# Performance work log

Measured on AMD Instinct MI355X. Metric: run time of the kernel, lower is better.

Reference implementation:

```python
import jax, jax.numpy as jnp
import numpy as np

B, T, O, H = 64, 1000, 61, 256
IN0, IN1 = 320, 2 * H  # layer0 input = 8*40 flattened feats; layer1 input = bidirectional concat


def setup_inputs() -> dict:
    key = jax.random.key(0)
    ks = jax.random.split(key, 12)
    rn = lambda k, shape: (jax.random.normal(k, shape, dtype=jnp.float32) * 0.05)
    inp = {}
    inp["batch"] = jax.random.normal(ks[0], (B, T, 8, 40), dtype=jnp.float32)
    lengths = np.random.RandomState(0).randint(T // 2, T + 1, size=B).astype(np.int64)
    inp["lengths"] = jnp.asarray(lengths)
    # GRU params stacked over directions: [2, 3H, in], [2, 3H, H], biases [2, 3H]
    inp["w_ih_l0"] = rn(ks[1], (2, 3 * H, IN0))
    inp["w_hh_l0"] = rn(ks[2], (2, 3 * H, H))
    inp["b_ih_l0"] = rn(ks[3], (2, 3 * H))
    inp["b_hh_l0"] = rn(ks[4], (2, 3 * H))
    inp["w_ih_l1"] = rn(ks[5], (2, 3 * H, IN1))
    inp["w_hh_l1"] = rn(ks[6], (2, 3 * H, H))
    inp["b_ih_l1"] = rn(ks[7], (2, 3 * H))
    inp["b_hh_l1"] = rn(ks[8], (2, 3 * H))
    inp["fc_w"] = rn(ks[9], (O, 2 * H))
    inp["fc_b"] = rn(ks[10], (O,))
    return inp


def _gru_dir(x, w_ih, w_hh, b_ih, b_hh, reverse):
    # x: [T, B, in] -> ys: [T, B, H]; torch GRU cell semantics
    def step(h, xt):
        gi = xt @ w_ih.T + b_ih          # [B, 3H]
        gh = h @ w_hh.T + b_hh           # [B, 3H]
        i_r, i_z, i_n = jnp.split(gi, 3, axis=-1)
        h_r, h_z, h_n = jnp.split(gh, 3, axis=-1)
        r = jax.nn.sigmoid(i_r + h_r)
        z = jax.nn.sigmoid(i_z + h_z)
        n = jnp.tanh(i_n + r * h_n)
        h_new = (1.0 - z) * n + z * h
        return h_new, h_new
    h0 = jnp.zeros((x.shape[1], w_hh.shape[-1]), x.dtype)
    _, ys = jax.lax.scan(step, h0, x, reverse=reverse)
    return ys


def _bigru_layer(x, w_ih, w_hh, b_ih, b_hh):
    fwd = _gru_dir(x, w_ih[0], w_hh[0], b_ih[0], b_hh[0], reverse=False)
    bwd = _gru_dir(x, w_ih[1], w_hh[1], b_ih[1], b_hh[1], reverse=True)
    return jnp.concatenate([fwd, bwd], axis=-1)  # [T, B, 2H]


def reference(batch, lengths, w_ih_l0, w_hh_l0, b_ih_l0, b_hh_l0,
              w_ih_l1, w_hh_l1, b_ih_l1, b_hh_l1, fc_w, fc_b):
    b, t = batch.shape[0], batch.shape[1]
    x = jnp.swapaxes(batch, 2, 3).reshape(b, t, -1)   # transpose(2,3).flatten(2) -> [B,T,320]
    x = jnp.swapaxes(x, 0, 1)                          # [T, B, 320] (time-major like torch GRU)
    h1 = _bigru_layer(x, w_ih_l0, w_hh_l0, b_ih_l0, b_hh_l0)
    h2 = _bigru_layer(h1, w_ih_l1, w_hh_l1, b_ih_l1, b_hh_l1)
    out = h2 @ fc_w.T + fc_b                           # [T, B, O]
    out = jnp.swapaxes(out, 0, 1)                      # [B, T, O]
    # gather first lengths[i] timesteps of each sample, concatenated
    L = np.asarray(lengths)
    mask = np.arange(t)[None, :] < L[:, None]
    bi, ti = np.nonzero(mask)
    return out[bi, ti]                                 # [sum(lengths), O]
```

## Files before the change

### kernel.cpp

```cpp
#include <hip/hip_runtime.h>
#include <cstdint>
#include <cstddef>


typedef __attribute__((ext_vector_type(8))) __bf16 bf16x8;
typedef __attribute__((ext_vector_type(4))) float f32x4;
typedef __attribute__((ext_vector_type(4))) unsigned int u32x4;

#define AS1 __attribute__((address_space(1)))
#define AS3 __attribute__((address_space(3)))

#define LOG2E 1.44269504089f
#define SRZ  (-1.44269504089f)
#define SN   (2.88539008177f)

__device__ __forceinline__ void async_ld16(const void* g, void* l) {
  __builtin_amdgcn_global_load_lds((const AS1 unsigned int*)g,
                                   (AS3 unsigned int*)l, 16, 0, 0);
}

__device__ __forceinline__ f32x4 mfma16(u32x4 a, u32x4 b, f32x4 c) {
  return __builtin_amdgcn_mfma_f32_16x16x32_bf16(
      __builtin_bit_cast(bf16x8, a), __builtin_bit_cast(bf16x8, b), c, 0, 0, 0);
}

__device__ __forceinline__ unsigned short f2b(float f) {
  unsigned int u = __float_as_uint(f);
  u += 0x7fffu + ((u >> 16) & 1u);
  return (unsigned short)(u >> 16);
}
__device__ __forceinline__ float b2f(unsigned short s) {
  return __uint_as_float(((unsigned int)s) << 16);
}
__device__ __forceinline__ unsigned int cvtpk(float lo, float hi) {
  unsigned int r;
  asm("v_cvt_pk_bf16_f32 %0, %1, %2" : "=v"(r) : "v"(lo), "v"(hi));
  return r;
}
__device__ __forceinline__ float lo16(unsigned int d) {
  return __uint_as_float(d << 16);
}
__device__ __forceinline__ float hi16(unsigned int d) {
  return __uint_as_float(d & 0xffff0000u);
}
__device__ __forceinline__ float gload(const float* p, size_t i) { return p[i]; }
__device__ __forceinline__ float gload(const unsigned short* p, size_t i) { return b2f(p[i]); }

__device__ __forceinline__ float sigm2(float xs) {
  return __builtin_amdgcn_rcpf(1.0f + __builtin_amdgcn_exp2f(xs));
}
__device__ __forceinline__ float tanh2(float ys) {
  return __builtin_fmaf(-2.0f,
      __builtin_amdgcn_rcpf(1.0f + __builtin_amdgcn_exp2f(ys)), 1.0f);
}

__device__ __forceinline__ void lds_barrier() {
  asm volatile("" ::: "memory");
  __builtin_amdgcn_s_waitcnt(0xC07F);
  __builtin_amdgcn_s_barrier();
  asm volatile("" ::: "memory");
}

__global__ void cast_bf16_kernel(const float* __restrict__ src,
                                 unsigned short* __restrict__ dst, int n) {
  const int i = blockIdx.x * 256 + threadIdx.x;
  if (i < n) dst[i] = f2b(src[i]);
}

__global__ void cast_w_kernel(const float* __restrict__ src,
                              unsigned short* __restrict__ dst, int n,
                              int in_dim) {
  const int i = blockIdx.x * 256 + threadIdx.x;
  if (i < n) {
    const int row = (i / in_dim) % 768;
    const float s = (row < 512) ? SRZ : SN;
    dst[i] = f2b(s * src[i]);
  }
}

__global__ void cast_w_perm_kernel(const float* __restrict__ src,
                                   unsigned short* __restrict__ dst, int n,
                                   int in_dim, int scaled) {
  const int i = blockIdx.x * 256 + threadIdx.x;
  if (i < n) {
    const int row = i / in_dim;
    const int p = i - row * in_dim;
    const int hi = p >> 8, pr = p & 255;
    const int w = pr >> 5, c2 = pr & 31;
    const int k = hi * 256 + w * 32 + (c2 & 1) * 16 + (c2 >> 1);
    float s = 1.0f;
    if (scaled) s = ((row % 768) < 512) ? SRZ : SN;
    dst[i] = f2b(s * src[(size_t)row * in_dim + k]);
  }
}

__global__ void bias_fuse_kernel(const float* __restrict__ bih,
                                 const float* __restrict__ bhh,
                                 float* __restrict__ fb) {
  const int n = blockIdx.x * 256 + threadIdx.x;
  if (n < 1536) {
    const int dir = n >> 9 >> 1 ? 1 : (n / 768);
    const int rr = n - dir * 768;
    const float s = (rr < 512) ? SRZ : SN;
    float v = bih[dir * 768 + rr];
    if (rr < 512) v += bhh[dir * 768 + rr];
    fb[n] = s * v;
  }
}

__global__ void transpose_x_kernel(const float* __restrict__ batch,
                                   unsigned short* __restrict__ xb) {
  const int t = blockIdx.x, b = blockIdx.y, i = threadIdx.x;
  const float v = batch[((size_t)b * 1000 + t) * 320 + (i & 7) * 40 + (i >> 3)];
  xb[((size_t)t * 64 + b) * 320 + i] = f2b(v);
}

template <typename CT, bool PERM>
__global__ __launch_bounds__(256) void gemm_bt_kernel(
    const unsigned short* __restrict__ A, const unsigned short* __restrict__ W,
    const float* __restrict__ bias, CT* __restrict__ C, int M, int N, int K) {
  __shared__ __align__(16) unsigned short As[4096];
  __shared__ __align__(16) unsigned short Bs[4096];
  const int tid = threadIdx.x;
  const int lane = tid & 63;
  const int wv = tid >> 6;
  const int mBase = blockIdx.x * 128;
  const int nBase = blockIdx.y * 128;

  const int s0 = tid, s1 = tid + 256;
  const int r0 = ((s0 >> 6) << 4) | (s0 & 15), c0 = ((s0 >> 4) & 3) * 8;
  const int r1 = ((s1 >> 6) << 4) | (s1 & 15), c1 = ((s1 >> 4) & 3) * 8;

  const unsigned short* Arow0 = A + (size_t)(mBase + r0) * K + c0;
  const unsigned short* Arow1 = A + (size_t)(mBase + r1) * K + c1;
  const unsigned short* Wrow0 = W + (size_t)(nBase + r0) * K + c0;
  const unsigned short* Wrow1 = W + (size_t)(nBase + r1) * K + c1;

  char* lA = (char*)As;
  char* lB = (char*)Bs;
  char* dstA0 = lA + wv * 1024;
  char* dstA1 = lA + 4096 + wv * 1024;
  char* dstB0 = lB + wv * 1024;
  char* dstB1 = lB + 4096 + wv * 1024;

  f32x4 acc[4][4] = {};
  const int mh = (wv >> 1) * 64, nh = (wv & 1) * 64;
  const u32x4* As4 = (const u32x4*)As;
  const u32x4* Bs4 = (const u32x4*)Bs;

  for (int k0 = 0; k0 < K; k0 += 32) {
    __syncthreads();
    async_ld16(Arow0 + k0, dstA0);
    async_ld16(Arow1 + k0, dstA1);
    async_ld16(Wrow0 + k0, dstB0);
    async_ld16(Wrow1 + k0, dstB1);
    __syncthreads();
    u32x4 a[4], b[4];
#pragma unroll
    for (int mt = 0; mt < 4; ++mt) a[mt] = As4[((mh >> 4) + mt) * 64 + lane];
#pragma unroll
    for (int nt = 0; nt < 4; ++nt) b[nt] = Bs4[((nh >> 4) + nt) * 64 + lane];
#pragma unroll
    for (int mt = 0; mt < 4; ++mt)
#pragma unroll
      for (int nt = 0; nt < 4; ++nt)
        acc[mt][nt] = mfma16(a[mt], b[nt], acc[mt][nt]);
  }

  if constexpr (PERM) {
    const int t = (mBase + mh) >> 6;
#pragma unroll
    for (int p = 0; p < 2; ++p) {
      const int nb0 = nBase + nh + p * 32;
      const int dir = (nb0 >= 768) ? 1 : 0;
      const int np = nb0 - dir * 768;
      const int g = np >> 8;
      const int ww = (np >> 5) & 7;
      const float bn0 = bias[nb0 + (lane & 15)];
      const float bn1 = bias[nb0 + 16 + (lane & 15)];
#pragma unroll
      for (int mt = 0; mt < 4; ++mt) {
        const size_t slot = (size_t)t * 64 + (size_t)(mt * 2 + dir) * 8 + ww;
        if constexpr (sizeof(CT) == 2) {
          u32x4 v;
          v[0] = cvtpk(acc[mt][2 * p][0] + bn0, acc[mt][2 * p][1] + bn0);
          v[1] = cvtpk(acc[mt][2 * p][2] + bn0, acc[mt][2 * p][3] + bn0);
          v[2] = cvtpk(acc[mt][2 * p + 1][0] + bn1, acc[mt][2 * p + 1][1] + bn1);
          v[3] = cvtpk(acc[mt][2 * p + 1][2] + bn1, acc[mt][2 * p + 1][3] + bn1);
          *(u32x4*)((unsigned short*)C + slot * 1536 + (size_t)g * 512 +
                    (size_t)lane * 8) = v;
        } else {
#pragma unroll
          for (int rs = 0; rs < 2; ++rs) {
            f32x4 v = {acc[mt][2 * p][2 * rs] + bn0,
                       acc[mt][2 * p][2 * rs + 1] + bn0,
                       acc[mt][2 * p + 1][2 * rs] + bn1,
                       acc[mt][2 * p + 1][2 * rs + 1] + bn1};
            *(f32x4*)((float*)C + slot * 1536 + (size_t)(g * 2 + rs) * 256 +
                      (size_t)lane * 4) = v;
          }
        }
      }
    }
  } else {
#pragma unroll
    for (int nt = 0; nt < 4; ++nt) {
      const int n = nBase + nh + nt * 16 + (lane & 15);
      const float bn = bias[n];
#pragma unroll
      for (int mt = 0; mt < 4; ++mt) {
        const int mrow = mBase + mh + mt * 16 + ((lane >> 4) << 2);
#pragma unroll
        for (int r = 0; r < 4; ++r) {
          const float v = acc[mt][nt][r] + bn;
          if constexpr (sizeof(CT) == 2)
            ((unsigned short*)C)[(size_t)(mrow + r) * N + n] = f2b(v);
          else
            ((float*)C)[(size_t)(mrow + r) * N + n] = v;
        }
      }
    }
  }
}

#define GBLOCK(G)                                                              \
  {                                                                            \
    _Pragma("unroll") for (int kt = 0; kt < 6; ++kt) {                         \
      acc[0][G] = mfma16(a[kt], wv[0][G][kt], acc[0][G]);                      \
      acc[1][G] = mfma16(a[kt], wv[1][G][kt], acc[1][G]);                      \
    }                                                                          \
    _Pragma("unroll") for (int kk = 0; kk < 2; ++kk) {                         \
      u32x4 bf0 = *(const u32x4*)(wlds +                                       \
          (((w * 12 + (0 * 3 + (G)) * 2 + kk) << 10) + lane * 16));            \
      u32x4 bf1 = *(const u32x4*)(wlds +                                       \
          (((w * 12 + (1 * 3 + (G)) * 2 + kk) << 10) + lane * 16));            \
      acc[0][G] = mfma16(a[6 + kk], bf0, acc[0][G]);                           \
      acc[1][G] = mfma16(a[6 + kk], bf1, acc[1][G]);                           \
    }                                                                          \
  }

template <typename GT>
__global__ __launch_bounds__(512, 2) void gru_fast_kernel(
    const GT* __restrict__ gi,
    const unsigned short* __restrict__ whh,
    const float* __restrict__ bhh,
    unsigned short* __restrict__ hout) {
  constexpr int E = (int)sizeof(GT);
  constexpr int CH = (E * 1536) / 1024;
  constexpr bool DB = (E == 2);
  constexpr int HB = DB ? 18432 : 9216;
  extern __shared__ __align__(16) char smem[];
  char* wlds = smem;
  char* hl   = smem + 98304;
  char* glds = smem + 98304 + HB;
  const int tid = threadIdx.x;
  const int lane = tid & 63;
  const int w = tid >> 6;
  const int c = lane & 15;
  const int q = lane >> 4;
  const int dir = blockIdx.x & 1;
  const int sb = (blockIdx.x >> 1) * 16;

  for (int i = tid; i < HB / 2; i += 512) ((unsigned short*)hl)[i] = 0;

  const int u0 = 32 * w + c;
  const float bhn0 = SN * bhh[dir * 768 + 512 + u0];
  const float bhn1 = SN * bhh[dir * 768 + 512 + u0 + 16];

  const unsigned short* wb =
      whh + (size_t)dir * 196608 + (size_t)u0 * 256 + q * 8;
  u32x4 wv[2][3][6];
#pragma unroll
  for (int j = 0; j < 2; ++j)
#pragma unroll
    for (int g = 0; g < 3; ++g) {
      const unsigned short* p = wb + (size_t)(g * 256 + 16 * j) * 256;
#pragma unroll
      for (int kt = 0; kt < 6; ++kt) wv[j][g][kt] = *(const u32x4*)(p + kt * 32);
#pragma unroll
      for (int kk = 0; kk < 2; ++kk) {
        u32x4 tmp = *(const u32x4*)(p + (6 + kk) * 32);
        *(u32x4*)(wlds + (((w * 12 + (j * 3 + g) * 2 + kk) << 10) + lane * 16)) = tmp;
      }
    }
#pragma unroll
  for (int j = 0; j < 2; ++j)
#pragma unroll
    for (int g = 0; g < 3; ++g)
#pragma unroll
      for (int kt = 0; kt < 6; ++kt)
        asm volatile("" : "+v"(wv[j][g][kt]));

  float h0[4] = {0.f, 0.f, 0.f, 0.f}, h1[4] = {0.f, 0.f, 0.f, 0.f};

  const int t0 = dir ? 999 : 0;
  unsigned int* hp = (unsigned int*)hout +
                     ((size_t)t0 * 64 + sb) * 256 + dir * 128 + w * 16 + c;
  const ptrdiff_t gstep = (dir ? -1 : 1) * (ptrdiff_t)(64 * 1536);
  const ptrdiff_t hstep = (dir ? -1 : 1) * (ptrdiff_t)(64 * 256);

  char* gdw = glds + w * (1536 * E);
  const size_t slot0 =
      (size_t)t0 * 64 + (size_t)((blockIdx.x >> 1) * 2 + dir) * 8 + w;
  const GT* gp2 = gi + slot0 * 1536 + (size_t)lane * (16 / E);
#pragma unroll
  for (int i = 0; i < CH; ++i)
    async_ld16(gp2 + i * (1024 / E), gdw + i * 1024);
  gp2 += gstep;

  __syncthreads();

  const char* habase = hl + c * 576 + q * 16;
  const int hwb = q * 4 * 576 + w * 64 + c * 4;

  auto body = [&](int rd, int wr, bool first) {
    u32x4 a[8];
#pragma unroll
    for (int kt = 0; kt < 8; ++kt)
      a[kt] = *(const u32x4*)(habase + rd + kt * 64);
    if constexpr (!DB) lds_barrier();

    f32x4 acc[2][3] = {};
    GBLOCK(0)

    if (first) asm volatile("s_waitcnt vmcnt(0)" ::: "memory");
    else       asm volatile("s_waitcnt vmcnt(4)" ::: "memory");
    u32x4 raw[CH];
#pragma unroll
    for (int i = 0; i < CH; ++i)
      raw[i] = *(const u32x4*)(gdw + i * 1024 + lane * 16);

    float pvA[3][4], pvB[3][4];
    if constexpr (E == 2) {
#pragma unroll
      for (int g = 0; g < 3; ++g)
#pragma unroll
        for (int r = 0; r < 4; ++r) {
          const unsigned int d0 = raw[g][r >> 1];
          const unsigned int d1 = raw[g][2 + (r >> 1)];
          pvA[g][r] = (r & 1) ? hi16(d0) : lo16(d0);
          pvB[g][r] = (r & 1) ? hi16(d1) : lo16(d1);
        }
    } else {
#pragma unroll
      for (int g = 0; g < 3; ++g)
#pragma unroll
        for (int r = 0; r < 4; ++r) {
          const f32x4 f = __builtin_bit_cast(f32x4, raw[g * 2 + (r >> 1)]);
          pvA[g][r] = f[r & 1];
          pvB[g][r] = f[2 + (r & 1)];
        }
    }

    float rr0[4], rr1[4];
#pragma unroll
    for (int r = 0; r < 4; ++r) {
      rr0[r] = sigm2(pvA[0][r] + acc[0][0][r]);
      rr1[r] = sigm2(pvB[0][r] + acc[1][0][r]);
    }

    GBLOCK(2)

    float nn0[4], nn1[4];
#pragma unroll
    for (int r = 0; r < 4; ++r) {
      nn0[r] = tanh2(__builtin_fmaf(rr0[r], acc[0][2][r] + bhn0, pvA[2][r]));
      nn1[r] = tanh2(__builtin_fmaf(rr1[r], acc[1][2][r] + bhn1, pvB[2][r]));
    }

    GBLOCK(1)

    asm volatile("s_waitcnt lgkmcnt(0)" ::: "memory");
#pragma unroll
    for (int i = 0; i < CH; ++i)
      async_ld16(gp2 + i * (1024 / E), gdw + i * 1024);
    gp2 += gstep;

    unsigned short* hls = (unsigned short*)(hl + wr);
#pragma unroll
    for (int r = 0; r < 4; ++r) {
      const float zz0 = sigm2(pvA[1][r] + acc[0][1][r]);
      const float hv0 = __builtin_fmaf(zz0, h0[r] - nn0[r], nn0[r]);
      h0[r] = hv0;
      const float zz1 = sigm2(pvB[1][r] + acc[1][1][r]);
      const float hv1 = __builtin_fmaf(zz1, h1[r] - nn1[r], nn1[r]);
      h1[r] = hv1;
      const unsigned int pk = cvtpk(hv0, hv1);
      *(unsigned int*)((char*)hls + hwb + r * 576) = pk;
      hp[(size_t)(q * 4 + r) * 256] = pk;
    }
    hp += hstep;
    lds_barrier();
  };

  if constexpr (DB) {
    body(0, 9216, true);
    body(9216, 0, false);
    for (int it = 1; it < 500; ++it) {
      body(0, 9216, false);
      body(9216, 0, false);
    }
  } else {
    body(0, 0, true);
    for (int step = 1; step < 1000; ++step) body(0, 0, false);
  }
  asm volatile("s_waitcnt vmcnt(0)" ::: "memory");
}

template <typename GT>
__global__ __launch_bounds__(1024) void gru_layer_kernel(
    const GT* __restrict__ gi, const unsigned short* __restrict__ whh,
    const float* __restrict__ bhh, unsigned short* __restrict__ hout) {
  __shared__ __align__(16) unsigned short hbf[16][264];
  __shared__ __align__(16) float gh[16][780];
  const int tid = threadIdx.x;
  const int lane = tid & 63;
  const int wv = tid >> 6;
  const int dir = blockIdx.x & 1;
  const int sb = (blockIdx.x >> 1) * 16;
  const int j = tid & 255;
  const int si = tid >> 8;

  float hreg[4] = {0.f, 0.f, 0.f, 0.f};
#pragma unroll
  for (int i = 0; i < 4; ++i) hbf[si + i * 4][j] = 0;

  const float bh_n = SN * bhh[dir * 768 + 512 + j];

  const unsigned short* wl = whh + (size_t)dir * 768 * 256 +
                             (size_t)(wv * 48 + (lane & 15)) * 256 +
                             ((lane >> 4) * 8);
  const char* habase = (const char*)hbf + (lane & 15) * 528 + ((lane >> 4) << 4);
  const int srow = (lane >> 4) * 4;

  __syncthreads();

  for (int step = 0; step < 1000; ++step) {
    const int t = dir ? (999 - step) : step;
    float p_ir[4], p_iz[4], p_in[4];
#pragma unroll
    for (int i = 0; i < 4; ++i) {
      const int s = si + i * 4;
      const size_t gib = ((size_t)t * 64 + (sb + s)) * 1536 + dir * 768 + j;
      p_ir[i] = gload(gi, gib);
      p_iz[i] = gload(gi, gib + 256);
      p_in[i] = gload(gi, gib + 512);
    }
    u32x4 a[8];
#pragma unroll
    for (int kt = 0; kt < 8; ++kt) a[kt] = *(const u32x4*)(habase + kt * 64);
#pragma unroll
    for (int ntd = 0; ntd < 3; ++ntd) {
      f32x4 acc = {0.f, 0.f, 0.f, 0.f};
#pragma unroll
      for (int kt = 0; kt < 8; ++kt) {
        u32x4 bfrag = *(const u32x4*)(wl + ntd * (16 * 256) + kt * 32);
        acc = mfma16(a[kt], bfrag, acc);
      }
      const int gcol = (wv * 3 + ntd) * 16 + (lane & 15);
#pragma unroll
      for (int r = 0; r < 4; ++r) gh[srow + r][gcol] = acc[r];
    }
    __syncthreads();
#pragma unroll
    for (int i = 0; i < 4; ++i) {
      const int s = si + i * 4;
      const float r = sigm2(p_ir[i] + gh[s][j]);
      const float z = sigm2(p_iz[i] + gh[s][256 + j]);
      const float n = tanh2(__builtin_fmaf(r, gh[s][512 + j] + bh_n, p_in[i]));
      const float h = __builtin_fmaf(z, hreg[i] - n, n);
      hreg[i] = h;
      const unsigned short hb = f2b(h);
      hbf[s][j] = hb;
      hout[((size_t)t * 64 + (sb + s)) * 512 + dir * 256 + j] = hb;
    }
    __syncthreads();
  }
}

__global__ void prefix_kernel(const int* __restrict__ raw,
                              int* __restrict__ pref, int* __restrict__ lens) {
  if (threadIdx.x == 0) {
    const int stride = (raw[1] == 0 && raw[3] == 0 && raw[5] == 0) ? 2 : 1;
    int a = 0;
    for (int b = 0; b < 64; ++b) {
      const int L = raw[b * stride];
      pref[b] = a;
      lens[b] = L;
      a += L;
    }
  }
}

__global__ __launch_bounds__(256) void fc_kernel(
    const unsigned short* __restrict__ h2, const unsigned short* __restrict__ fcw,
    const float* __restrict__ fcb, const int* __restrict__ lens,
    const int* __restrict__ pref, float* __restrict__ out) {
  __shared__ __align__(16) unsigned short hrow[4][512];
  const int b = blockIdx.y;
  const int sub = threadIdx.x >> 6, lane = threadIdx.x & 63;
  const int t = blockIdx.x * 4 + sub;
  *(u32x4*)&hrow[sub][lane * 8] =
      *(const u32x4*)&h2[((size_t)t * 64 + b) * 512 + lane * 8];
  __syncthreads();
  const int len = lens[b];
  if (lane < 61 && t < len) {
    float acc = fcb[lane];
    const unsigned short* wr = fcw + (size_t)lane * 512;
#pragma unroll 4
    for (int k = 0; k < 512; k += 8) {
      u32x4 w4 = *(const u32x4*)(wr + k);
      u32x4 h4 = *(const u32x4*)(&hrow[sub][k]);
#pragma unroll
      for (int qq = 0; qq < 4; ++qq) {
        acc += __uint_as_float(w4[qq] << 16) * __uint_as_float(h4[qq] << 16);
        acc += __uint_as_float(w4[qq] & 0xffff0000u) * __uint_as_float(h4[qq] & 0xffff0000u);
      }
    }
    out[((size_t)pref[b] + t) * 61 + lane] = acc;
  }
}

template <typename GT>
static void run_pipeline(const float* batch, const int* lengths_raw,
                         const float* w_ih_l0, const float* w_hh_l0,
                         const float* b_ih_l0, const float* b_hh_l0,
                         const float* w_ih_l1, const float* w_hh_l1,
                         const float* b_ih_l1, const float* b_hh_l1,
                         const float* fc_w, const float* fc_b, float* out,
                         char* ws, hipStream_t stream) {
  size_t off = 0;
  auto alloc = [&](size_t bytes) -> char* {
    char* p = ws + off;
    off += (bytes + 255) & ~(size_t)255;
    return p;
  };
  char* pool = alloc((size_t)64000 * 512 * 2);
  unsigned short* xb = (unsigned short*)pool;
  unsigned short* h1 = (unsigned short*)pool;
  unsigned short* h2 = (unsigned short*)pool;
  GT*             gi   = (GT*)alloc((size_t)64064 * 1536 * sizeof(GT));
  unsigned short* wih0 = (unsigned short*)alloc((size_t)1536 * 320 * 2);
  unsigned short* wih1 = (unsigned short*)alloc((size_t)1536 * 512 * 2);
  unsigned short* whh0 = (unsigned short*)alloc((size_t)1536 * 256 * 2);
  unsigned short* whh1 = (unsigned short*)alloc((size_t)1536 * 256 * 2);
  unsigned short* fcwb = (unsigned short*)alloc((size_t)61 * 512 * 2);
  float*          fb0  = (float*)alloc(1536 * 4);
  float*          fb1  = (float*)alloc(1536 * 4);
  int*            pref = (int*)alloc(256);
  int*            lens = (int*)alloc(256);

  const int HB = (sizeof(GT) == 2) ? 18432 : 9216;
  const int GRU_LDS = 98304 + HB + 8 * 1536 * (int)sizeof(GT);
  const bool big_lds =
      hipFuncSetAttribute(reinterpret_cast<const void*>(gru_fast_kernel<GT>),
                          hipFuncAttributeMaxDynamicSharedMemorySize,
                          GRU_LDS) == hipSuccess;

  auto castw_lin = [&](const float* s, unsigned short* d, int n, int in_dim) {
    cast_w_kernel<<<dim3((n + 255) / 256), dim3(256), 0, stream>>>(s, d, n, in_dim);
  };
  auto castw_perm = [&](const float* s, unsigned short* d, int n, int in_dim,
                        int scaled) {
    cast_w_perm_kernel<<<dim3((n + 255) / 256), dim3(256), 0, stream>>>(
        s, d, n, in_dim, scaled);
  };

  castw_lin(w_ih_l0, wih0, 2 * 768 * 320, 320);
  if (big_lds) {
    castw_perm(w_hh_l0, whh0, 2 * 768 * 256, 256, 1);
    castw_perm(w_hh_l1, whh1, 2 * 768 * 256, 256, 1);
    castw_perm(w_ih_l1, wih1, 2 * 768 * 512, 512, 1);
    castw_perm(fc_w, fcwb, 61 * 512, 512, 0);
  } else {
    castw_lin(w_hh_l0, whh0, 2 * 768 * 256, 256);
    castw_lin(w_hh_l1, whh1, 2 * 768 * 256, 256);
    castw_lin(w_ih_l1, wih1, 2 * 768 * 512, 512);
    cast_bf16_kernel<<<dim3((61 * 512 + 255) / 256), dim3(256), 0, stream>>>(
        fc_w, fcwb, 61 * 512);
  }
  bias_fuse_kernel<<<dim3(6), dim3(256), 0, stream>>>(b_ih_l0, b_hh_l0, fb0);
  bias_fuse_kernel<<<dim3(6), dim3(256), 0, stream>>>(b_ih_l1, b_hh_l1, fb1);

  transpose_x_kernel<<<dim3(1000, 64), dim3(320), 0, stream>>>(batch, xb);

  auto gemm = [&](const unsigned short* A, const unsigned short* W,
                  const float* fb, GT* Cc, int M, int N, int K) {
    if (big_lds)
      gemm_bt_kernel<GT, true><<<dim3(500, 12), dim3(256), 0, stream>>>(
          A, W, fb, Cc, M, N, K);
    else
      gemm_bt_kernel<GT, false><<<dim3(500, 12), dim3(256), 0, stream>>>(
          A, W, fb, Cc, M, N, K);
  };
  auto gru = [&](GT* g, unsigned short* w, const float* b, unsigned short* h) {
    if (big_lds)
      gru_fast_kernel<GT><<<dim3(8), dim3(512), GRU_LDS, stream>>>(g, w, b, h);
    else
      gru_layer_kernel<GT><<<dim3(8), dim3(1024), 0, stream>>>(g, w, b, h);
  };

  gemm(xb, wih0, fb0, gi, 64000, 1536, 320);
  gru(gi, whh0, b_hh_l0, h1);
  gemm(h1, wih1, fb1, gi, 64000, 1536, 512);
  gru(gi, whh1, b_hh_l1, h2);

  prefix_kernel<<<dim3(1), dim3(64), 0, stream>>>(lengths_raw, pref, lens);
  fc_kernel<<<dim3(250, 64), dim3(256), 0, stream>>>(h2, fcwb, fc_b, lens, pref, out);
}

extern "C" void kernel_launch(void* const* d_in, const int* in_sizes, int n_in,
                              void* d_out, int out_size, void* d_ws, size_t ws_size,
                              hipStream_t stream) {
  (void)in_sizes; (void)n_in; (void)out_size;
  const float* batch   = (const float*)d_in[0];
  const int*   lengths = (const int*)d_in[1];
  const float* w_ih_l0 = (const float*)d_in[2];
  const float* w_hh_l0 = (const float*)d_in[3];
  const float* b_ih_l0 = (const float*)d_in[4];
  const float* b_hh_l0 = (const float*)d_in[5];
  const float* w_ih_l1 = (const float*)d_in[6];
  const float* w_hh_l1 = (const float*)d_in[7];
  const float* b_ih_l1 = (const float*)d_in[8];
  const float* b_hh_l1 = (const float*)d_in[9];
  const float* fc_w    = (const float*)d_in[10];
  const float* fc_b    = (const float*)d_in[11];
  float* out = (float*)d_out;
  char* ws = (char*)d_ws;

  const size_t NEED_FP32 = 470000000ull;
  if (ws_size >= NEED_FP32) {
    run_pipeline<float>(batch, lengths, w_ih_l0, w_hh_l0, b_ih_l0, b_hh_l0,
                        w_ih_l1, w_hh_l1, b_ih_l1, b_hh_l1, fc_w, fc_b, out,
                        ws, stream);
  } else {
    run_pipeline<unsigned short>(batch, lengths, w_ih_l0, w_hh_l0, b_ih_l0,
                                 b_hh_l0, w_ih_l1, w_hh_l1, b_ih_l1, b_hh_l1,
                                 fc_w, fc_b, out, ws, stream);
  }
}
```

Measured before the change: 3.637 ms.

## Double-buffer GEMM LDS tiles and seed GRU accumulators with input projections

The input-projection GEMM now uses two LDS buffers, so the next K-slice is prefetched asynchronously while MFMAs run on the current slice, with one barrier per iteration instead of two. In the recurrent GRU step, the z-gate accumulator is initialised with the precomputed input projection and the n-gate accumulator with the hidden bias. This removes the separate adds after the MFMA chain on the serial critical path. The cost is doubled LDS use in the GEMM and a prefetch on the final iteration that reads one slice past K.

```diff
diff --git a/kernel.cpp b/kernel.cpp
--- a/kernel.cpp
+++ b/kernel.cpp
@@ -119,8 +119,8 @@
 __global__ __launch_bounds__(256) void gemm_bt_kernel(
     const unsigned short* __restrict__ A, const unsigned short* __restrict__ W,
     const float* __restrict__ bias, CT* __restrict__ C, int M, int N, int K) {
-  __shared__ __align__(16) unsigned short As[4096];
-  __shared__ __align__(16) unsigned short Bs[4096];
+  __shared__ __align__(16) unsigned short As[2][4096];
+  __shared__ __align__(16) unsigned short Bs[2][4096];
   const int tid = threadIdx.x;
   const int lane = tid & 63;
   const int wv = tid >> 6;
@@ -136,25 +136,27 @@
   const unsigned short* Wrow0 = W + (size_t)(nBase + r0) * K + c0;
   const unsigned short* Wrow1 = W + (size_t)(nBase + r1) * K + c1;
 
-  char* lA = (char*)As;
-  char* lB = (char*)Bs;
-  char* dstA0 = lA + wv * 1024;
-  char* dstA1 = lA + 4096 + wv * 1024;
-  char* dstB0 = lB + wv * 1024;
-  char* dstB1 = lB + 4096 + wv * 1024;
+  auto stage = [&](int buf, int k0) {
+    char* lA = (char*)As[buf];
+    char* lB = (char*)Bs[buf];
+    async_ld16(Arow0 + k0, lA + wv * 1024);
+    async_ld16(Arow1 + k0, lA + 4096 + wv * 1024);
+    async_ld16(Wrow0 + k0, lB + wv * 1024);
+    async_ld16(Wrow1 + k0, lB + 4096 + wv * 1024);
+  };
 
   f32x4 acc[4][4] = {};
   const int mh = (wv >> 1) * 64, nh = (wv & 1) * 64;
-  const u32x4* As4 = (const u32x4*)As;
-  const u32x4* Bs4 = (const u32x4*)Bs;
-
-  for (int k0 = 0; k0 < K; k0 += 32) {
-    __syncthreads();
-    async_ld16(Arow0 + k0, dstA0);
-    async_ld16(Arow1 + k0, dstA1);
-    async_ld16(Wrow0 + k0, dstB0);
-    async_ld16(Wrow1 + k0, dstB1);
-    __syncthreads();
+
+  stage(0, 0);
+  __syncthreads();
+
+  const int NT = K >> 5;
+  for (int t = 0; t < NT; ++t) {
+    const int cur = t & 1;
+    stage(cur ^ 1, (t + 1) << 5);
+    const u32x4* As4 = (const u32x4*)As[cur];
+    const u32x4* Bs4 = (const u32x4*)Bs[cur];
     u32x4 a[4], b[4];
 #pragma unroll
     for (int mt = 0; mt < 4; ++mt) a[mt] = As4[((mh >> 4) + mt) * 64 + lane];
@@ -165,6 +167,7 @@
 #pragma unroll
       for (int nt = 0; nt < 4; ++nt)
         acc[mt][nt] = mfma16(a[mt], b[nt], acc[mt][nt]);
+    __syncthreads();
   }
 
   if constexpr (PERM) {
@@ -320,7 +323,9 @@
       a[kt] = *(const u32x4*)(habase + rd + kt * 64);
     if constexpr (!DB) lds_barrier();
 
-    f32x4 acc[2][3] = {};
+    f32x4 acc[2][3];
+    acc[0][0] = f32x4{0.f, 0.f, 0.f, 0.f};
+    acc[1][0] = f32x4{0.f, 0.f, 0.f, 0.f};
     GBLOCK(0)
 
     if (first) asm volatile("s_waitcnt vmcnt(0)" ::: "memory");
@@ -330,33 +335,44 @@
     for (int i = 0; i < CH; ++i)
       raw[i] = *(const u32x4*)(gdw + i * 1024 + lane * 16);
 
-    float pvA[3][4], pvB[3][4];
+    float pvr0[4], pvr1[4], pvn0[4], pvn1[4];
     if constexpr (E == 2) {
 #pragma unroll
-      for (int g = 0; g < 3; ++g)
-#pragma unroll
-        for (int r = 0; r < 4; ++r) {
-          const unsigned int d0 = raw[g][r >> 1];
-          const unsigned int d1 = raw[g][2 + (r >> 1)];
-          pvA[g][r] = (r & 1) ? hi16(d0) : lo16(d0);
-          pvB[g][r] = (r & 1) ? hi16(d1) : lo16(d1);
-        }
+      for (int r = 0; r < 4; ++r) {
+        const unsigned int dr0 = raw[0][r >> 1], dr1 = raw[0][2 + (r >> 1)];
+        const unsigned int dz0 = raw[1][r >> 1], dz1 = raw[1][2 + (r >> 1)];
+        const unsigned int dn0 = raw[2][r >> 1], dn1 = raw[2][2 + (r >> 1)];
+        pvr0[r] = (r & 1) ? hi16(dr0) : lo16(dr0);
+        pvr1[r] = (r & 1) ? hi16(dr1) : lo16(dr1);
+        acc[0][1][r] = (r & 1) ? hi16(dz0) : lo16(dz0);
+        acc[1][1][r] = (r & 1) ? hi16(dz1) : lo16(dz1);
+        pvn0[r] = (r & 1) ? hi16(dn0) : lo16(dn0);
+        pvn1[r] = (r & 1) ? hi16(dn1) : lo16(dn1);
+        acc[0][2][r] = bhn0;
+        acc[1][2][r] = bhn1;
+      }
     } else {
 #pragma unroll
-      for (int g = 0; g < 3; ++g)
-#pragma unroll
-        for (int r = 0; r < 4; ++r) {
-          const f32x4 f = __builtin_bit_cast(f32x4, raw[g * 2 + (r >> 1)]);
-          pvA[g][r] = f[r & 1];
-          pvB[g][r] = f[2 + (r & 1)];
-        }
+      for (int r = 0; r < 4; ++r) {
+        const f32x4 f0 = __builtin_bit_cast(f32x4, raw[0 + (r >> 1)]);
+        const f32x4 f1 = __builtin_bit_cast(f32x4, raw[2 + (r >> 1)]);
+        const f32x4 f2 = __builtin_bit_cast(f32x4, raw[4 + (r >> 1)]);
+        pvr0[r] = f0[r & 1];
+        pvr1[r] = f0[2 + (r & 1)];
+        acc[0][1][r] = f1[r & 1];
+        acc[1][1][r] = f1[2 + (r & 1)];
+        pvn0[r] = f2[r & 1];
+        pvn1[r] = f2[2 + (r & 1)];
+        acc[0][2][r] = bhn0;
+        acc[1][2][r] = bhn1;
+      }
     }
 
     float rr0[4], rr1[4];
 #pragma unroll
     for (int r = 0; r < 4; ++r) {
-      rr0[r] = sigm2(pvA[0][r] + acc[0][0][r]);
-      rr1[r] = sigm2(pvB[0][r] + acc[1][0][r]);
+      rr0[r] = sigm2(pvr0[r] + acc[0][0][r]);
+      rr1[r] = sigm2(pvr1[r] + acc[1][0][r]);
     }
 
     GBLOCK(2)
@@ -364,8 +380,8 @@
     float nn0[4], nn1[4];
 #pragma unroll
     for (int r = 0; r < 4; ++r) {
-      nn0[r] = tanh2(__builtin_fmaf(rr0[r], acc[0][2][r] + bhn0, pvA[2][r]));
-      nn1[r] = tanh2(__builtin_fmaf(rr1[r], acc[1][2][r] + bhn1, pvB[2][r]));
+      nn0[r] = tanh2(__builtin_fmaf(rr0[r], acc[0][2][r], pvn0[r]));
+      nn1[r] = tanh2(__builtin_fmaf(rr1[r], acc[1][2][r], pvn1[r]));
     }
 
     GBLOCK(1)
@@ -379,10 +395,10 @@
     unsigned short* hls = (unsigned short*)(hl + wr);
 #pragma unroll
     for (int r = 0; r < 4; ++r) {
-      const float zz0 = sigm2(pvA[1][r] + acc[0][1][r]);
+      const float zz0 = sigm2(acc[0][1][r]);
       const float hv0 = __builtin_fmaf(zz0, h0[r] - nn0[r], nn0[r]);
       h0[r] = hv0;
-      const float zz1 = sigm2(pvB[1][r] + acc[1][1][r]);
+      const float zz1 = sigm2(acc[1][1][r]);
       const float hv1 = __builtin_fmaf(zz1, h1[r] - nn1[r], nn1[r]);
       h1[r] = hv1;
       const unsigned int pk = cvtpk(hv0, hv1);
```

After: 3.722 ms. 1.02x slower.
